# Kernel optimization log

Hardware: AMD Instinct MI355X
Metric: run time of the kernel (lower is better)

Reference implementation:

```python
import jax, jax.numpy as jnp
import numpy as np
from jax import lax


def _crf_numerator(emissions, tags, mask, start_transitions, end_transitions, transitions):
    # emissions [B,S,L], tags [B,S] int, mask [B,S] bool
    B, S, L = emissions.shape
    em = jnp.take_along_axis(emissions, tags[..., None], axis=-1)[..., 0]  # [B,S]
    tr = transitions[tags[:, :-1], tags[:, 1:]]  # [B,S-1]
    m = mask.astype(emissions.dtype)
    score = start_transitions[tags[:, 0]] + em[:, 0]
    score = score + jnp.sum(m[:, 1:] * (tr + em[:, 1:]), axis=1)
    seq_len = jnp.sum(mask.astype(jnp.int32), axis=1)  # [B]
    last_tags = tags[jnp.arange(B), seq_len - 1]
    return score + end_transitions[last_tags]


def _crf_denominator(emissions, mask, start_transitions, end_transitions, transitions):
    # Forward algorithm (log-sum-exp recurrence) over time via lax.scan.
    score0 = start_transitions[None, :] + emissions[:, 0]  # [B,L]

    def step(score, inp):
        emit, m = inp  # emit [B,L], m [B] bool
        nxt = jax.nn.logsumexp(score[:, :, None] + transitions[None, :, :] + emit[:, None, :], axis=1)
        score = jnp.where(m[:, None], nxt, score)
        return score, None

    emits = jnp.swapaxes(emissions[:, 1:], 0, 1)  # [S-1,B,L]
    ms = jnp.swapaxes(mask[:, 1:], 0, 1)          # [S-1,B]
    score, _ = lax.scan(step, score0, (emits, ms))
    return jax.nn.logsumexp(score + end_transitions[None, :], axis=1)


def setup_inputs() -> dict:
    key = jax.random.key(0)
    ks = jax.random.split(key, 6)
    B, S, H, L = 32, 2048, 1024, 13
    hidden_states = jax.random.normal(ks[0], (B, S, H), jnp.float32)
    attention_mask = jnp.ones((B, S), jnp.int32)
    labels = jax.random.randint(ks[1], (B, S), 0, L, dtype=jnp.int32)
    W = jax.random.normal(ks[2], (L, H), jnp.float32) * 0.02
    b = jnp.zeros((L,), jnp.float32)
    start_transitions = jax.random.uniform(ks[3], (L,), jnp.float32, -0.1, 0.1)
    end_transitions = jax.random.uniform(ks[4], (L,), jnp.float32, -0.1, 0.1)
    transitions = jax.random.uniform(ks[5], (L, L), jnp.float32, -0.1, 0.1)
    return dict(hidden_states=hidden_states, attention_mask=attention_mask, labels=labels,
                W=W, b=b, start_transitions=start_transitions,
                end_transitions=end_transitions, transitions=transitions)


def reference(hidden_states, attention_mask, labels, W, b, start_transitions, end_transitions, transitions):
    # classifier (dropout omitted: eval mode / deterministic)
    logits = jnp.einsum('bsh,lh->bsl', hidden_states, W) + b  # [B,S,L]
    mask = attention_mask.astype(bool)
    num = _crf_numerator(logits, labels, mask, start_transitions, end_transitions, transitions)
    den = _crf_denominator(logits, mask, start_transitions, end_transitions, transitions)
    llh = num - den  # [B]
    loss = -jnp.mean(llh)  # reduction='mean', negated
    return loss, logits
```

## Files before the change

kernel.cpp:

```cpp
#include <hip/hip_runtime.h>
#include <math.h>

#define Lc 13
#define Hc 1024
#define Bc 32
#define Sc 2048
#define BSc (Bc*Sc)
#define CHUNK 128
#define NCHUNK 16
#define NBLK (Bc*NCHUNK)

#define NSTRIPE 1024
#define GRID_A  768

#define INV_LN2 1.44269504088896340736f
#define LN2f    0.69314718055994530942f

#if __has_builtin(__builtin_amdgcn_exp2f)
#define EXP2F(x) __builtin_amdgcn_exp2f(x)
#else
#define EXP2F(x) exp2f(x)
#endif
#if __has_builtin(__builtin_amdgcn_logf)
#define LOG2F(x) __builtin_amdgcn_logf(x)
#else
#define LOG2F(x) log2f(x)
#endif

template <int CTRL>
__device__ __forceinline__ float dpp_add(float v) {
  int p = __builtin_amdgcn_update_dpp(0, __float_as_int(v), CTRL, 0xF, 0xF, true);
  return v + __int_as_float(p);
}

__global__ __launch_bounds__(512, 6)
void k_logits(const float* __restrict__ A, const float* __restrict__ W,
              const float* __restrict__ bias, float* __restrict__ out) {
  __shared__ float Wl[Lc * Hc];
  const int tid = threadIdx.x;
  const int ln  = tid & 63;
  const int wv  = tid >> 6;
  const int rin = ln >> 4;
  const int ch  = ln & 15;

  for (int stripe = blockIdx.x; stripe < NSTRIPE; stripe += GRID_A) {
    const size_t rowBase = (size_t)stripe * 64 + (size_t)wv * 8;
    const float* A0 = A + (rowBase + rin) * (size_t)Hc + ch * 4;
    const float* A1 = A0 + 4 * (size_t)Hc;

    float4 buf00 = *(const float4*)(A0);
    float4 buf10 = *(const float4*)(A1);
    float4 buf01 = *(const float4*)(A0 + 64);
    float4 buf11 = *(const float4*)(A1 + 64);
    __builtin_amdgcn_sched_barrier(0);

    if (stripe == (int)blockIdx.x) {
      const float4* Wg4 = (const float4*)W;
      float4* Wl4 = (float4*)Wl;
#pragma unroll
      for (int i = 0; i < 7; ++i) {
        int idx = tid + i * 512;
        if (idx < Lc * (Hc / 4)) Wl4[idx] = Wg4[idx];
      }
      __syncthreads();
    }

    float acc0[Lc], acc1[Lc];
#pragma unroll
    for (int l = 0; l < Lc; ++l) { acc0[l] = 0.f; acc1[l] = 0.f; }

    float4 buf02, buf12;
#pragma unroll
    for (int kk = 0; kk < 16; ++kk) {
      float4 a0 = (kk % 3 == 0) ? buf00 : (kk % 3 == 1) ? buf01 : buf02;
      float4 a1 = (kk % 3 == 0) ? buf10 : (kk % 3 == 1) ? buf11 : buf12;
      if (kk + 2 < 16) {
        float4 n0 = *(const float4*)(A0 + (kk + 2) * 64);
        float4 n1 = *(const float4*)(A1 + (kk + 2) * 64);
        if ((kk + 2) % 3 == 0)      { buf00 = n0; buf10 = n1; }
        else if ((kk + 2) % 3 == 1) { buf01 = n0; buf11 = n1; }
        else                        { buf02 = n0; buf12 = n1; }
      }
      const float* wb = &Wl[kk * 64 + ch * 4];
#pragma unroll
      for (int l = 0; l < Lc; ++l) {
        float4 w = *(const float4*)(wb + l * Hc);
        acc0[l] = fmaf(a0.x, w.x, acc0[l]); acc0[l] = fmaf(a0.y, w.y, acc0[l]);
        acc0[l] = fmaf(a0.z, w.z, acc0[l]); acc0[l] = fmaf(a0.w, w.w, acc0[l]);
        acc1[l] = fmaf(a1.x, w.x, acc1[l]); acc1[l] = fmaf(a1.y, w.y, acc1[l]);
        acc1[l] = fmaf(a1.z, w.z, acc1[l]); acc1[l] = fmaf(a1.w, w.w, acc1[l]);
      }
    }

#pragma unroll
    for (int l = 0; l < Lc; ++l) {
      float s0 = acc0[l], s1 = acc1[l];
      s0 = dpp_add<0xB1>(s0);   s1 = dpp_add<0xB1>(s1);
      s0 = dpp_add<0x4E>(s0);   s1 = dpp_add<0x4E>(s1);
      s0 = dpp_add<0x141>(s0);  s1 = dpp_add<0x141>(s1);
      s0 = dpp_add<0x140>(s0);  s1 = dpp_add<0x140>(s1);
      acc0[l] = s0; acc1[l] = s1;
    }
    float ov0 = 0.f, ov1 = 0.f;
#pragma unroll
    for (int l = 0; l < Lc; ++l) {
      float bl = bias[l];
      ov0 = (ch == l) ? acc0[l] + bl : ov0;
      ov1 = (ch == l) ? acc1[l] + bl : ov1;
    }
    if (ch < Lc) {
      out[(rowBase + rin) * Lc + ch]     = ov0;
      out[(rowBase + 4 + rin) * Lc + ch] = ov1;
    }
  }
}

__global__ void k_chunks(const float* __restrict__ logits, const int* __restrict__ mask,
                         const int* __restrict__ labels, const float* __restrict__ T,
                         float* __restrict__ Mout, float* __restrict__ numpart,
                         float* __restrict__ cntpart, float* __restrict__ out0) {
  const int bp = blockIdx.x;
  const int b  = bp >> 4;
  const int p  = bp & 15;
  const int tid = threadIdx.x;
  if (bp == 0 && tid == 0) out0[0] = 0.f;
  const int g = tid >> 4;
  const int k = tid & 15;
  const int kk = (k < 13) ? k : 0;
  const int gg = (g < 13) ? g : 0;
  const bool active = (g < 13) && (k < 13);
  const size_t lbase = (size_t)b * Sc;
  const int t0 = 1 + p * CHUNK;
  const int t1 = min(t0 + CHUNK, Sc);

  float U[13];
#pragma unroll
  for (int j = 0; j < 13; ++j) U[j] = EXP2F(T[j * 13 + kk] * INV_LN2);

  float e0 = logits[(lbase + t0) * Lc + kk] * INV_LN2;
  int   m0 = mask[lbase + t0];
  float P = m0 ? EXP2F(T[gg * 13 + kk] * INV_LN2 + e0) : ((g == k) ? 1.f : 0.f);
  float off = 0.f;

  for (int t = t0 + 1; t < t1; ++t) {
    float e2 = logits[(lbase + t) * Lc + kk] * INV_LN2;
    int   mk = mask[lbase + t];
    float pj[13];
#pragma unroll
    for (int j = 0; j < 13; ++j) pj[j] = __shfl(P, j, 16);
    float s0 = pj[0] * U[0];  s0 = fmaf(pj[4],  U[4],  s0);
    s0 = fmaf(pj[8],  U[8],  s0);  s0 = fmaf(pj[12], U[12], s0);
    float s1 = pj[1] * U[1];  s1 = fmaf(pj[5],  U[5],  s1);  s1 = fmaf(pj[9],  U[9],  s1);
    float s2 = pj[2] * U[2];  s2 = fmaf(pj[6],  U[6],  s2);  s2 = fmaf(pj[10], U[10], s2);
    float s3 = pj[3] * U[3];  s3 = fmaf(pj[7],  U[7],  s3);  s3 = fmaf(pj[11], U[11], s3);
    float s = (s0 + s1) + (s2 + s3);
    float Pn = EXP2F(e2) * s;
    P = mk ? Pn : P;
    if (((t - t0) & 7) == 0) {
      float mx = P;
#pragma unroll
      for (int o = 1; o < 16; o <<= 1) mx = fmaxf(mx, __shfl_xor(mx, o, 16));
      unsigned eb = (__float_as_uint(mx) >> 23) & 255u;
      float scale = __uint_as_float((254u - eb) << 23);
      P *= scale;
      off += (float)((int)eb - 127);
    }
  }
  if (active) Mout[(size_t)bp * 169 + g * 13 + k] = (P > 0.f) ? (LOG2F(P) + off) : -1e30f;

  if (tid < 64) {
    float np = 0.f; int cnt = 0;
    for (int t = t0 + tid; t < t1; t += 64) {
      int mk = mask[lbase + t];
      if (mk) {
        int tg = labels[lbase + t];
        int pg = labels[lbase + t - 1];
        np += T[pg * 13 + tg] + logits[(lbase + t) * Lc + tg];
        cnt += 1;
      }
    }
#pragma unroll
    for (int o = 1; o < 64; o <<= 1) {
      np  += __shfl_xor(np, o, 64);
      cnt += __shfl_xor(cnt, o, 64);
    }
    if (tid == 0) { numpart[bp] = np; cntpart[bp] = (float)cnt; }
  }
}

__global__ void k_final(const float* __restrict__ logits, const int* __restrict__ mask,
                        const int* __restrict__ labels, const float* __restrict__ startT,
                        const float* __restrict__ endT, const float* __restrict__ Mws,
                        const float* __restrict__ numpart, const float* __restrict__ cntpart,
                        float* __restrict__ out0) {
  const int b = blockIdx.x;
  const int lane = threadIdx.x;
  const int kk = (lane < 13) ? lane : 0;
  const size_t lbase = (size_t)b * Sc;

  float v = (startT[kk] + logits[lbase * Lc + kk]) * INV_LN2;
  for (int p = 0; p < NCHUNK; ++p) {
    const float* Mp = Mws + (size_t)(b * NCHUNK + p) * 169;
    float a[13];
#pragma unroll
    for (int j = 0; j < 13; ++j) a[j] = __shfl(v, j, 64) + Mp[j * 13 + kk];
    float mx = a[0];
#pragma unroll
    for (int j = 1; j < 13; ++j) mx = fmaxf(mx, a[j]);
    float s = 0.f;
#pragma unroll
    for (int j = 0; j < 13; ++j) s += EXP2F(a[j] - mx);
    v = mx + LOG2F(s);
  }
  float x = (lane < 13) ? (v + endT[kk] * INV_LN2) : -1e30f;
  float mx = x;
#pragma unroll
  for (int off = 1; off < 16; off <<= 1) mx = fmaxf(mx, __shfl_xor(mx, off, 16));
  float sx = EXP2F(x - mx);
#pragma unroll
  for (int off = 1; off < 16; off <<= 1) sx += __shfl_xor(sx, off, 16);
  float den = (mx + LOG2F(sx)) * LN2f;

  float np = 0.f, cs = 0.f;
  if (lane < NCHUNK) { np = numpart[b * NCHUNK + lane]; cs = cntpart[b * NCHUNK + lane]; }
#pragma unroll
  for (int o = 1; o < 16; o <<= 1) {
    np += __shfl_xor(np, o, 16);
    cs += __shfl_xor(cs, o, 16);
  }
  if (lane == 0) {
    int lab0 = labels[lbase];
    int seqlen = mask[lbase] + (int)(cs + 0.5f);
    int lastTag = labels[lbase + seqlen - 1];
    float num = startT[lab0] + logits[lbase * Lc + lab0] + np + endT[lastTag];
    float llh = num - den;
    atomicAdd(out0, -llh * (1.0f / Bc));
  }
}

extern "C" void kernel_launch(void* const* d_in, const int* in_sizes, int n_in,
                              void* d_out, int out_size, void* d_ws, size_t ws_size,
                              hipStream_t stream) {
  const float* hs     = (const float*)d_in[0];
  const int*   amask  = (const int*)d_in[1];
  const int*   labels = (const int*)d_in[2];
  const float* W      = (const float*)d_in[3];
  const float* bias   = (const float*)d_in[4];
  const float* startT = (const float*)d_in[5];
  const float* endT   = (const float*)d_in[6];
  const float* T      = (const float*)d_in[7];

  float* out    = (float*)d_out;
  float* logits = out + 1;
  float* Mws    = (float*)d_ws;
  float* numpart = Mws + (size_t)NBLK * 169;
  float* cntpart = numpart + NBLK;

  k_logits<<<GRID_A, 512, 0, stream>>>(hs, W, bias, logits);
  k_chunks<<<NBLK, 256, 0, stream>>>(logits, amask, labels, T, Mws, numpart, cntpart, out);
  k_final <<<Bc, 64, 0, stream>>>(logits, amask, labels, startT, endT, Mws, numpart, cntpart, out);
}
```

Measured before the change: 108.1 us.

## Store classifier weights as bf16 in LDS and launch one block per stripe

The logits kernel now rounds W to bf16 (round-to-nearest-even) while staging it into shared memory, halving LDS footprint and the bytes read per weight fetch. W is unpacked back to fp32 for the FMAs. The persistent grid-stride loop over stripes is replaced by a grid of one block per 64-row stripe, and every block stages its own copy of W. This lowers weight precision in the logits output, and the per-block staging and conversion work may offset the smaller LDS footprint.

```diff
diff --git a/kernel.cpp b/kernel.cpp
--- a/kernel.cpp
+++ b/kernel.cpp
@@ -10,8 +10,7 @@
 #define NCHUNK 16
 #define NBLK (Bc*NCHUNK)
 
-#define NSTRIPE 1024
-#define GRID_A  768
+#define WU32   (Lc*512)
 
 #define INV_LN2 1.44269504088896340736f
 #define LN2f    0.69314718055994530942f
@@ -36,82 +35,87 @@
 __global__ __launch_bounds__(512, 6)
 void k_logits(const float* __restrict__ A, const float* __restrict__ W,
               const float* __restrict__ bias, float* __restrict__ out) {
-  __shared__ float Wl[Lc * Hc];
+  __shared__ unsigned Wb[WU32];
   const int tid = threadIdx.x;
   const int ln  = tid & 63;
   const int wv  = tid >> 6;
   const int rin = ln >> 4;
   const int ch  = ln & 15;
-
-  for (int stripe = blockIdx.x; stripe < NSTRIPE; stripe += GRID_A) {
-    const size_t rowBase = (size_t)stripe * 64 + (size_t)wv * 8;
-    const float* A0 = A + (rowBase + rin) * (size_t)Hc + ch * 4;
-    const float* A1 = A0 + 4 * (size_t)Hc;
-
-    float4 buf00 = *(const float4*)(A0);
-    float4 buf10 = *(const float4*)(A1);
-    float4 buf01 = *(const float4*)(A0 + 64);
-    float4 buf11 = *(const float4*)(A1 + 64);
-    __builtin_amdgcn_sched_barrier(0);
-
-    if (stripe == (int)blockIdx.x) {
-      const float4* Wg4 = (const float4*)W;
-      float4* Wl4 = (float4*)Wl;
-#pragma unroll
-      for (int i = 0; i < 7; ++i) {
-        int idx = tid + i * 512;
-        if (idx < Lc * (Hc / 4)) Wl4[idx] = Wg4[idx];
-      }
-      __syncthreads();
-    }
-
-    float acc0[Lc], acc1[Lc];
-#pragma unroll
-    for (int l = 0; l < Lc; ++l) { acc0[l] = 0.f; acc1[l] = 0.f; }
-
-    float4 buf02, buf12;
-#pragma unroll
-    for (int kk = 0; kk < 16; ++kk) {
-      float4 a0 = (kk % 3 == 0) ? buf00 : (kk % 3 == 1) ? buf01 : buf02;
-      float4 a1 = (kk % 3 == 0) ? buf10 : (kk % 3 == 1) ? buf11 : buf12;
-      if (kk + 2 < 16) {
-        float4 n0 = *(const float4*)(A0 + (kk + 2) * 64);
-        float4 n1 = *(const float4*)(A1 + (kk + 2) * 64);
-        if ((kk + 2) % 3 == 0)      { buf00 = n0; buf10 = n1; }
-        else if ((kk + 2) % 3 == 1) { buf01 = n0; buf11 = n1; }
-        else                        { buf02 = n0; buf12 = n1; }
-      }
-      const float* wb = &Wl[kk * 64 + ch * 4];
-#pragma unroll
-      for (int l = 0; l < Lc; ++l) {
-        float4 w = *(const float4*)(wb + l * Hc);
-        acc0[l] = fmaf(a0.x, w.x, acc0[l]); acc0[l] = fmaf(a0.y, w.y, acc0[l]);
-        acc0[l] = fmaf(a0.z, w.z, acc0[l]); acc0[l] = fmaf(a0.w, w.w, acc0[l]);
-        acc1[l] = fmaf(a1.x, w.x, acc1[l]); acc1[l] = fmaf(a1.y, w.y, acc1[l]);
-        acc1[l] = fmaf(a1.z, w.z, acc1[l]); acc1[l] = fmaf(a1.w, w.w, acc1[l]);
-      }
-    }
-
+  const size_t rowBase = (size_t)blockIdx.x * 64 + (size_t)wv * 8;
+
+  const float* A0 = A + (rowBase + rin) * (size_t)Hc + ch * 4;
+  const float* A1 = A0 + 4 * (size_t)Hc;
+
+  float4 buf00 = *(const float4*)(A0);
+  float4 buf10 = *(const float4*)(A1);
+  float4 buf01 = *(const float4*)(A0 + 64);
+  float4 buf11 = *(const float4*)(A1 + 64);
+  __builtin_amdgcn_sched_barrier(0);
+
+  {
+    const unsigned* Wg = (const unsigned*)W;
+#pragma unroll
+    for (int i = 0; i < 13; ++i) {
+      int j = tid + i * 512;
+      unsigned x0 = Wg[2 * j];
+      unsigned x1 = Wg[2 * j + 1];
+      unsigned r0 = (x0 + 0x7FFFu + ((x0 >> 16) & 1u)) >> 16;
+      unsigned r1 = (x1 + 0x7FFFu + ((x1 >> 16) & 1u)) >> 16;
+      Wb[j] = r0 | (r1 << 16);
+    }
+  }
+  __syncthreads();
+
+  float acc0[Lc], acc1[Lc];
+#pragma unroll
+  for (int l = 0; l < Lc; ++l) { acc0[l] = 0.f; acc1[l] = 0.f; }
+
+  float4 buf02, buf12;
+#pragma unroll
+  for (int kk = 0; kk < 16; ++kk) {
+    float4 a0 = (kk % 3 == 0) ? buf00 : (kk % 3 == 1) ? buf01 : buf02;
+    float4 a1 = (kk % 3 == 0) ? buf10 : (kk % 3 == 1) ? buf11 : buf12;
+    if (kk + 2 < 16) {
+      float4 n0 = *(const float4*)(A0 + (kk + 2) * 64);
+      float4 n1 = *(const float4*)(A1 + (kk + 2) * 64);
+      if ((kk + 2) % 3 == 0)      { buf00 = n0; buf10 = n1; }
+      else if ((kk + 2) % 3 == 1) { buf01 = n0; buf11 = n1; }
+      else                        { buf02 = n0; buf12 = n1; }
+    }
+    const unsigned* wq = &Wb[kk * 32 + ch * 2];
 #pragma unroll
     for (int l = 0; l < Lc; ++l) {
-      float s0 = acc0[l], s1 = acc1[l];
-      s0 = dpp_add<0xB1>(s0);   s1 = dpp_add<0xB1>(s1);
-      s0 = dpp_add<0x4E>(s0);   s1 = dpp_add<0x4E>(s1);
-      s0 = dpp_add<0x141>(s0);  s1 = dpp_add<0x141>(s1);
-      s0 = dpp_add<0x140>(s0);  s1 = dpp_add<0x140>(s1);
-      acc0[l] = s0; acc1[l] = s1;
-    }
-    float ov0 = 0.f, ov1 = 0.f;
-#pragma unroll
-    for (int l = 0; l < Lc; ++l) {
-      float bl = bias[l];
-      ov0 = (ch == l) ? acc0[l] + bl : ov0;
-      ov1 = (ch == l) ? acc1[l] + bl : ov1;
-    }
-    if (ch < Lc) {
-      out[(rowBase + rin) * Lc + ch]     = ov0;
-      out[(rowBase + 4 + rin) * Lc + ch] = ov1;
-    }
+      uint2 wp = *(const uint2*)(wq + l * 512);
+      float w0 = __uint_as_float(wp.x << 16);
+      float w1 = __uint_as_float(wp.x & 0xffff0000u);
+      float w2 = __uint_as_float(wp.y << 16);
+      float w3 = __uint_as_float(wp.y & 0xffff0000u);
+      acc0[l] = fmaf(a0.x, w0, acc0[l]); acc0[l] = fmaf(a0.y, w1, acc0[l]);
+      acc0[l] = fmaf(a0.z, w2, acc0[l]); acc0[l] = fmaf(a0.w, w3, acc0[l]);
+      acc1[l] = fmaf(a1.x, w0, acc1[l]); acc1[l] = fmaf(a1.y, w1, acc1[l]);
+      acc1[l] = fmaf(a1.z, w2, acc1[l]); acc1[l] = fmaf(a1.w, w3, acc1[l]);
+    }
+  }
+
+#pragma unroll
+  for (int l = 0; l < Lc; ++l) {
+    float s0 = acc0[l], s1 = acc1[l];
+    s0 = dpp_add<0xB1>(s0);   s1 = dpp_add<0xB1>(s1);
+    s0 = dpp_add<0x4E>(s0);   s1 = dpp_add<0x4E>(s1);
+    s0 = dpp_add<0x141>(s0);  s1 = dpp_add<0x141>(s1);
+    s0 = dpp_add<0x140>(s0);  s1 = dpp_add<0x140>(s1);
+    acc0[l] = s0; acc1[l] = s1;
+  }
+  float ov0 = 0.f, ov1 = 0.f;
+#pragma unroll
+  for (int l = 0; l < Lc; ++l) {
+    float bl = bias[l];
+    ov0 = (ch == l) ? acc0[l] + bl : ov0;
+    ov1 = (ch == l) ? acc1[l] + bl : ov1;
+  }
+  if (ch < Lc) {
+    out[(rowBase + rin) * Lc + ch]     = ov0;
+    out[(rowBase + 4 + rin) * Lc + ch] = ov1;
   }
 }
 
@@ -256,7 +260,7 @@
   float* numpart = Mws + (size_t)NBLK * 169;
   float* cntpart = numpart + NBLK;
 
-  k_logits<<<GRID_A, 512, 0, stream>>>(hs, W, bias, logits);
+  k_logits<<<BSc / 64, 512, 0, stream>>>(hs, W, bias, logits);
   k_chunks<<<NBLK, 256, 0, stream>>>(logits, amask, labels, T, Mws, numpart, cntpart, out);
   k_final <<<Bc, 64, 0, stream>>>(logits, amask, labels, startT, endT, Mws, numpart, cntpart, out);
 }
```

Result: slower. 282.9 us (+161.8%).
